# Kernel tuning notes

Measured on AMD Instinct MI355X. Metric: run time of the kernel, lower is better.

Reference implementation:

```python
import jax, jax.numpy as jnp
import numpy as np
from jax import lax

EPS = 1e-5
QUANT_BITS = 16  # Conv2dShift default input fixed-point bits


def round_fixed(x, quant_bits=QUANT_BITS):
    # fixed-point rounding of activations with straight-through estimator
    scale = 2.0 ** (quant_bits - 1)
    xq = jnp.round(x * scale) / scale
    return x + lax.stop_gradient(xq - x)


def shift_conv3x3(x, w_shift, stride=1):
    # w_shift already holds sign * 2^shift power-of-two weights (see setup)
    x = round_fixed(x)
    return lax.conv_general_dilated(
        x, w_shift, window_strides=(stride, stride), padding=[(1, 1), (1, 1)],
        dimension_numbers=("NCHW", "OIHW", "NCHW"))


def adder_conv3x3(x, w):
    # AdderNet: out[n,co,h,w] = -sum_{ci,kh,kw} |patch - w[co,ci,kh,kw]|
    Co = w.shape[0]
    # patches: [N, C*3*3, H, W], feature ordering (c, kh, kw) matches w.reshape
    p = lax.conv_general_dilated_patches(
        x, filter_shape=(3, 3), window_strides=(1, 1), padding=[(1, 1), (1, 1)])
    wf = w.reshape(Co, -1)

    def per_out_channel(wc):  # wc: [C*9]
        return -jnp.sum(jnp.abs(p - wc[None, :, None, None]), axis=1)  # [N,H,W]

    out = lax.map(per_out_channel, wf)  # [Co, N, H, W] (sequential: bounds memory)
    return jnp.transpose(out, (1, 0, 2, 3))


def batch_norm(x, gamma, beta):
    # training-mode BN (batch statistics), matching nn.BatchNorm2d default forward
    m = jnp.mean(x, axis=(0, 2, 3), keepdims=True)
    v = jnp.var(x, axis=(0, 2, 3), keepdims=True)
    xn = (x - m) * lax.rsqrt(v + EPS)
    return xn * gamma.reshape(1, -1, 1, 1) + beta.reshape(1, -1, 1, 1)


def _quantize_shift_weights(w, weight_bits=5):
    # DeepShift PS: weight -> sign * 2^round(log2|w|), shift clipped
    sign = jnp.where(w >= 0, 1.0, -1.0)
    shift = jnp.round(jnp.log2(jnp.abs(w) + 1e-12))
    shift = jnp.clip(shift, -(2.0 ** (weight_bits - 1) - 1.0), 0.0)
    return sign * jnp.exp2(shift)


def setup_inputs() -> dict:
    key = jax.random.key(0)
    ks = jax.random.split(key, 9)
    N, C, H, W = 64, 128, 32, 32
    planes = 128
    fan = 1.0 / np.sqrt(C * 9)
    x = jax.random.normal(ks[0], (N, C, H, W), dtype=jnp.float32)
    w_shift1 = _quantize_shift_weights(
        jax.random.normal(ks[1], (planes, C, 3, 3), dtype=jnp.float32) * fan)
    w_add1 = jax.random.normal(ks[2], (planes, planes, 3, 3), dtype=jnp.float32) * fan
    w_shift2 = _quantize_shift_weights(
        jax.random.normal(ks[3], (planes, planes, 3, 3), dtype=jnp.float32) * fan)
    w_add2 = jax.random.normal(ks[4], (planes, planes, 3, 3), dtype=jnp.float32) * fan
    gamma1 = jnp.ones((planes,), jnp.float32)
    beta1 = jnp.zeros((planes,), jnp.float32)
    gamma2 = jnp.ones((planes,), jnp.float32)
    beta2 = jnp.zeros((planes,), jnp.float32)
    return {"x": x, "w_shift1": w_shift1, "w_add1": w_add1, "gamma1": gamma1,
            "beta1": beta1, "w_shift2": w_shift2, "w_add2": w_add2,
            "gamma2": gamma2, "beta2": beta2}


def reference(x, w_shift1, w_add1, gamma1, beta1, w_shift2, w_add2, gamma2, beta2):
    residual = x
    out = shift_conv3x3(x, w_shift1, stride=1)
    out = adder_conv3x3(out, w_add1)
    out = jax.nn.relu(batch_norm(out, gamma1, beta1))
    out = shift_conv3x3(out, w_shift2, stride=1)
    out = adder_conv3x3(out, w_add2)
    out = batch_norm(out, gamma2, beta2)
    out = jax.nn.relu(out + residual)
    return out
```

## Files before the change

kernel.cpp:

```cpp
#include <hip/hip_runtime.h>


#define NB   64
#define CIN  128
#define HW   32
#define COUT 128
constexpr int PLANE    = HW * HW;
constexpr int NPAIR    = CIN / 2;
constexpr int CI_CHUNK = 4;
constexpr int CO_CHUNK = 8;
constexpr int LPLANE   = 34 * 32;
constexpr int LDS_TOT  = 2 * CI_CHUNK * LPLANE;
constexpr int A_CO     = 4;
constexpr float FSCALE    = 32768.0f;
constexpr float INV_SCALE = 1.0f / 32768.0f;
constexpr float QS     = 2048.0f;
constexpr float QB     = 32768.5f;
constexpr float INV_QS = 1.0f / 2048.0f;
constexpr unsigned PZ  = 0x80008000u;

constexpr int G_ROWB   = 32 * 4 * 16;
constexpr int G_CIQB   = 34 * G_ROWB;
constexpr int G_NB     = 4 * G_CIQB;

typedef _Float16 f16x8 __attribute__((ext_vector_type(8)));
typedef float    f32x4 __attribute__((ext_vector_type(4)));

#define GLOBAL_AS __attribute__((address_space(1)))
#define LDS_AS    __attribute__((address_space(3)))

__device__ __forceinline__ int fsw(int w) { return (w & 3) ^ ((w >> 2) & 3); }

__device__ __forceinline__ void gload_lds16(const void* g, void* l) {
    __builtin_amdgcn_global_load_lds((const GLOBAL_AS void*)g, (LDS_AS void*)l,
                                     16, 0, 0);
}
__device__ __forceinline__ float dpp_prev(float x) {
    return __int_as_float(__builtin_amdgcn_update_dpp(
        0, __float_as_int(x), 0x111, 0xF, 0xF, true));
}
__device__ __forceinline__ float dpp_next(float x) {
    return __int_as_float(__builtin_amdgcn_update_dpp(
        0, __float_as_int(x), 0x101, 0xF, 0xF, true));
}
__device__ __forceinline__ unsigned dpp_prev_u(unsigned x) {
    return (unsigned)__builtin_amdgcn_update_dpp(0, (int)x, 0x111, 0xF, 0xF, true);
}
__device__ __forceinline__ unsigned dpp_next_u(unsigned x) {
    return (unsigned)__builtin_amdgcn_update_dpp(0, (int)x, 0x101, 0xF, 0xF, true);
}
__device__ __forceinline__ uint4 dpp4_shr(uint4 v) {
    uint4 r;
    r.x = dpp_prev_u(v.x); r.y = dpp_prev_u(v.y);
    r.z = dpp_prev_u(v.z); r.w = dpp_prev_u(v.w);
    return r;
}
__device__ __forceinline__ uint4 dpp4_shl(uint4 v) {
    uint4 r;
    r.x = dpp_next_u(v.x); r.y = dpp_next_u(v.y);
    r.z = dpp_next_u(v.z); r.w = dpp_next_u(v.w);
    return r;
}
__device__ __forceinline__ void stage_plane4(const void* src, void* dst, int lane) {
#pragma unroll
    for (int i = 0; i < 4; ++i)
        gload_lds16((const char*)src + i * 1024 + lane * 16,
                    (char*)dst + 128 + i * 1024);
}
__device__ __forceinline__ unsigned q16(float a) {
    float t = fmaf(a, QS, QB);
    t = fminf(fmaxf(t, 0.0f), 65535.0f);
    return (unsigned)t;
}
__device__ __forceinline__ unsigned short f16b(float v) {
    return __builtin_bit_cast(unsigned short, (_Float16)v);
}

template <int WITH_BN>
__global__ __launch_bounds__(256) void transform_split(
    const float* __restrict__ in, const float* __restrict__ scale,
    const float* __restrict__ bias, uint4* __restrict__ G)
{
    __shared__ float sT[32 * 132];
    const int tid = threadIdx.x;
    const int b   = blockIdx.x;
    const int n   = b >> 5;
    const int ciq = (b >> 3) & 3;
    const int rq  = b & 7;

#pragma unroll
    for (int it = 0; it < 4; ++it) {
        int flat = it * 256 + tid;
        int ci_rel = flat >> 5;
        int px4 = (flat & 31) * 4;
        const float* ap = in + ((size_t)(n * CIN + ciq * 32 + ci_rel)) * PLANE
                             + rq * 128 + px4;
        float4 v = *reinterpret_cast<const float4*>(ap);
        if (WITH_BN) {
            float sc = scale[ciq * 32 + ci_rel], bs = bias[ciq * 32 + ci_rel];
            v.x = fmaxf(fmaf(v.x, sc, bs), 0.0f);
            v.y = fmaxf(fmaf(v.y, sc, bs), 0.0f);
            v.z = fmaxf(fmaf(v.z, sc, bs), 0.0f);
            v.w = fmaxf(fmaf(v.w, sc, bs), 0.0f);
        }
        v.x = rintf(v.x * FSCALE) * INV_SCALE;
        v.y = rintf(v.y * FSCALE) * INV_SCALE;
        v.z = rintf(v.z * FSCALE) * INV_SCALE;
        v.w = rintf(v.w * FSCALE) * INV_SCALE;
        *reinterpret_cast<float4*>(&sT[ci_rel * 132 + px4]) = v;
    }
    __syncthreads();

    uint4* Gp = G + ((size_t)n * G_NB + ciq * G_CIQB) / 16;
#pragma unroll
    for (int it = 0; it < 2; ++it) {
        int f = it * 256 + tid;
        int row_loc = f >> 7;
        int rem = f & 127;
        int w  = rem >> 2;
        int sg = rem & 3;
        int g  = sg ^ fsw(w);
        uint4 u;
        unsigned* up = &u.x;
#pragma unroll
        for (int j2 = 0; j2 < 4; ++j2) {
            unsigned lo = f16b(sT[(g * 8 + 2 * j2)     * 132 + row_loc * 32 + w]);
            unsigned hi = f16b(sT[(g * 8 + 2 * j2 + 1) * 132 + row_loc * 32 + w]);
            up[j2] = lo | (hi << 16);
        }
        int gr = rq * 4 + row_loc + 1;
        Gp[(gr * 32 + w) * 4 + sg] = u;
    }
    if (rq == 0 && tid < 128) Gp[tid] = make_uint4(0, 0, 0, 0);
    if (rq == 7 && tid < 128) Gp[33 * 128 + tid] = make_uint4(0, 0, 0, 0);
}

__global__ __launch_bounds__(256) void prep_weights(
    const float* __restrict__ a1, const float* __restrict__ a2,
    const float* __restrict__ s1w, const float* __restrict__ s2w,
    unsigned* __restrict__ wqo, unsigned* __restrict__ WFd,
    double* __restrict__ st)
{
    int i = blockIdx.x * 256 + threadIdx.x;
    if (blockIdx.x == 0) {
        st[threadIdx.x] = 0.0; st[threadIdx.x + 256] = 0.0;
    }
    if (i < 147456) {
        int layer = i >= 73728;
        int j   = i - layer * 73728;
        int co  = j / 576;
        int rem = j - co * 576;
        int cp  = rem / 9;
        int tap = rem - cp * 9;
        const float* w = layer ? a2 : a1;
        float f0 = w[((size_t)co * CIN + 2 * cp) * 9 + tap];
        float f1 = w[((size_t)co * CIN + 2 * cp + 1) * 9 + tap];
        wqo[i] = q16(f0) | (q16(f1) << 16);
    } else {
        int j = i - 147456;
        int layer = j >= 73728;
        int idx = j - layer * 73728;
        int j2  = idx & 3;
        int l   = (idx >> 2) & 63;
        int cot = (idx >> 8) & 7;
        int ciq = (idx >> 11) & 3;
        int tap = idx >> 13;
        int ci  = ciq * 32 + (l >> 4) * 8 + j2 * 2;
        int co  = cot * 16 + (l & 15);
        const float* w = layer ? s2w : s1w;
        unsigned lo = f16b(w[((size_t)co * CIN + ci) * 9 + tap]);
        unsigned hi = f16b(w[((size_t)co * CIN + ci + 1) * 9 + tap]);
        WFd[layer * 73728 + idx] = lo | (hi << 16);
    }
}

__global__ __launch_bounds__(256, 2) void conv_mfma(
    const uint4* __restrict__ G, const uint4* __restrict__ WF,
    unsigned* __restrict__ P)
{
    __shared__ uint4 sA[3072];
    const int tid  = threadIdx.x;
    const int lane = tid & 63;
    const int wid  = tid >> 6;
    const int b    = (blockIdx.x & 7) * 64 + (blockIdx.x >> 3);
    const int n    = b >> 3;
    const int q4   = b & 7;
    const int gsg  = lane >> 4;

    char* myL = (char*)sA + wid * 12288;
    const char* src = (const char*)G + (size_t)n * G_NB + (size_t)q4 * 4 * G_ROWB
                    + wid * 2048;

    f32x4 acc[8][2];
#pragma unroll
    for (int i = 0; i < 8; ++i)
#pragma unroll
        for (int j = 0; j < 2; ++j) acc[i][j] = (f32x4){0.f, 0.f, 0.f, 0.f};

    auto stage = [&](int ciq, int buf) {
        const char* s = src + ciq * G_CIQB;
#pragma unroll
        for (int rr = 0; rr < 3; ++rr)
#pragma unroll
            for (int k = 0; k < 2; ++k)
                gload_lds16(s + rr * 2048 + k * 1024 + lane * 16,
                            myL + buf * 6144 + rr * 2048 + k * 1024);
    };

    stage(0, 0);
    for (int ciq = 0; ciq < 4; ++ciq) {
        const int buf = ciq & 1;
        if (ciq < 3) {
            stage(ciq + 1, buf ^ 1);
            asm volatile("s_waitcnt vmcnt(6)" ::: "memory");
        } else {
            asm volatile("s_waitcnt vmcnt(0)" ::: "memory");
        }
        __builtin_amdgcn_sched_barrier(0);

        uint4 Brow[2][3];
        int pwh[2];
#pragma unroll
        for (int half = 0; half < 2; ++half) {
            pwh[half] = half * 16 + (lane & 15);
#pragma unroll
            for (int rr = 0; rr < 3; ++rr)
                Brow[half][rr] = *reinterpret_cast<const uint4*>(
                    myL + buf * 6144 + rr * 2048 + pwh[half] * 64
                    + ((gsg ^ fsw(pwh[half])) * 16));
        }
#pragma unroll
        for (int dh = 0; dh < 3; ++dh)
#pragma unroll
        for (int dw = 0; dw < 3; ++dw) {
            const uint4* wfp = WF + ((size_t)((dh * 3 + dw) * 4 + ciq)) * 512 + lane;
            f16x8 a[8];
#pragma unroll
            for (int cot = 0; cot < 8; ++cot)
                a[cot] = __builtin_bit_cast(f16x8, wfp[cot * 64]);
#pragma unroll
            for (int half = 0; half < 2; ++half) {
                uint4 braw;
                if (dw == 1) {
                    braw = Brow[half][dh];
                } else if (dw == 0) {
                    if (half == 0) braw = dpp4_shr(Brow[0][dh]);
                    else {
                        int w2 = pwh[1] - 1;
                        braw = *reinterpret_cast<const uint4*>(
                            myL + buf * 6144 + dh * 2048 + w2 * 64
                            + ((gsg ^ fsw(w2)) * 16));
                    }
                } else {
                    if (half == 1) braw = dpp4_shl(Brow[1][dh]);
                    else {
                        int w2 = pwh[0] + 1;
                        braw = *reinterpret_cast<const uint4*>(
                            myL + buf * 6144 + dh * 2048 + w2 * 64
                            + ((gsg ^ fsw(w2)) * 16));
                    }
                }
                f16x8 bf = __builtin_bit_cast(f16x8, braw);
#pragma unroll
                for (int cot = 0; cot < 8; ++cot)
                    acc[cot][half] = __builtin_amdgcn_mfma_f32_16x16x32_f16(
                        a[cot], bf, acc[cot][half], 0, 0, 0);
            }
        }
    }

    unsigned* Pn = P + (size_t)n * NPAIR * PLANE;
    const int r = q4 * 4 + wid;
#pragma unroll
    for (int cot = 0; cot < 8; ++cot) {
        int cp = cot * 8 + (lane >> 4) * 2;
#pragma unroll
        for (int p = 0; p < 2; ++p) {
            int px = r * 32 + p * 16 + (lane & 15);
            unsigned u01 = q16(acc[cot][p][0]) | (q16(acc[cot][p][1]) << 16);
            unsigned u23 = q16(acc[cot][p][2]) | (q16(acc[cot][p][3]) << 16);
            Pn[cp * PLANE + px] = u01;
            Pn[(cp + 1) * PLANE + px] = u23;
        }
    }
}

__global__ __launch_bounds__(256, 2) void conv_shift_valu(
    const float* __restrict__ in, const float* __restrict__ wgt,
    unsigned* __restrict__ out)
{
    __shared__ __align__(16) float sIn[LDS_TOT];
    const int tid  = threadIdx.x;
    const int lane = tid & 63;
    const int wid  = tid >> 6;
    const int bid  = (blockIdx.x & 7) * 128 + (blockIdx.x >> 3);
    const int n    = bid >> 4;
    const int co0  = (bid & 15) * CO_CHUNK;
    const int r    = tid >> 3;
    const int c    = tid & 7;
    const int c0   = c * 4;
    const bool cz  = (c == 0), c7 = (c == 7);

    float acc[4][CO_CHUNK];
#pragma unroll
    for (int p = 0; p < 4; ++p)
#pragma unroll
        for (int co = 0; co < CO_CHUNK; ++co) acc[p][co] = 0.0f;

    const float* inN = in + (size_t)n * CIN * PLANE;
    for (int idx = tid; idx < 512; idx += 256) {
        int slot = idx >> 6, wq = idx & 63;
        sIn[slot * LPLANE + (wq < 32 ? wq : 1024 + wq)] = 0.0f;
    }
    stage_plane4(inN + wid * PLANE, sIn + wid * LPLANE, lane);
    __syncthreads();

    int cur = 0;
    for (int ci0 = 0; ci0 < CIN; ci0 += CI_CHUNK) {
        if (ci0 + CI_CHUNK < CIN)
            stage_plane4(inN + (size_t)(ci0 + CI_CHUNK + wid) * PLANE,
                         sIn + ((cur ^ 1) * CI_CHUNK + wid) * LPLANE, lane);
        const float* sb = sIn + cur * CI_CHUNK * LPLANE;
#pragma unroll
        for (int cc = 0; cc < CI_CHUNK; ++cc) {
            float w[3][6];
#pragma unroll
            for (int dh = 0; dh < 3; ++dh) {
                const float* sp = sb + cc * LPLANE + (r + dh) * 32 + c0;
                float4 qv = *reinterpret_cast<const float4*>(sp);
                qv.x = rintf(qv.x * FSCALE) * INV_SCALE;
                qv.y = rintf(qv.y * FSCALE) * INV_SCALE;
                qv.z = rintf(qv.z * FSCALE) * INV_SCALE;
                qv.w = rintf(qv.w * FSCALE) * INV_SCALE;
                float lf = dpp_prev(qv.w);
                float rt = dpp_next(qv.x);
                w[dh][0] = cz ? 0.0f : lf;
                w[dh][1] = qv.x; w[dh][2] = qv.y; w[dh][3] = qv.z; w[dh][4] = qv.w;
                w[dh][5] = c7 ? 0.0f : rt;
            }
            const float* wp = wgt + ((size_t)co0 * CIN + (ci0 + cc)) * 9;
#pragma unroll
            for (int co = 0; co < CO_CHUNK; ++co)
#pragma unroll
                for (int dh = 0; dh < 3; ++dh)
#pragma unroll
                    for (int dw = 0; dw < 3; ++dw) {
                        const float wvv = wp[(size_t)co * CIN * 9 + dh * 3 + dw];
#pragma unroll
                        for (int p = 0; p < 4; ++p)
                            acc[p][co] = fmaf(w[dh][p + dw], wvv, acc[p][co]);
                    }
        }
        __syncthreads();
        cur ^= 1;
    }
    unsigned* outP = out + ((size_t)n * NPAIR + co0 / 2) * PLANE + r * HW + c0;
#pragma unroll
    for (int pr = 0; pr < CO_CHUNK / 2; ++pr) {
        uint4 v;
        unsigned* vp = &v.x;
#pragma unroll
        for (int p = 0; p < 4; ++p)
            vp[p] = q16(acc[p][2 * pr]) | (q16(acc[p][2 * pr + 1]) << 16);
        *reinterpret_cast<uint4*>(&outP[pr * PLANE]) = v;
    }
}

__global__ __launch_bounds__(256) void bn_relu_inplace(
    float4* __restrict__ io, const float* __restrict__ scale,
    const float* __restrict__ bias)
{
    int i = blockIdx.x * 256 + threadIdx.x;
    int c = (i >> 8) & 127;
    float sc = scale[c], bs = bias[c];
    float4 v = io[i];
    v.x = fmaxf(fmaf(v.x, sc, bs), 0.0f);
    v.y = fmaxf(fmaf(v.y, sc, bs), 0.0f);
    v.z = fmaxf(fmaf(v.z, sc, bs), 0.0f);
    v.w = fmaxf(fmaf(v.w, sc, bs), 0.0f);
    io[i] = v;
}

__global__ __launch_bounds__(256, 8) void adder_packed(
    const unsigned* __restrict__ in, const unsigned* __restrict__ wq,
    float* __restrict__ out, double* __restrict__ ssum, double* __restrict__ ssq)
{
    __shared__ __align__(16) unsigned sIn[4 * LPLANE];
    const int tid  = threadIdx.x;
    const int lane = tid & 63;
    const int wid  = tid >> 6;
    const int bid  = (blockIdx.x & 7) * 256 + (blockIdx.x >> 3);
    const int n    = bid >> 5;
    const int co0  = (bid & 31) * A_CO;
    const int r    = tid >> 3;
    const int c    = tid & 7;
    const int c0   = c * 4;
    const bool cz  = (c == 0), c7 = (c == 7);
    const unsigned pz = PZ;

    {
        int slot = tid >> 6, wqi = tid & 63;
        sIn[slot * LPLANE + (wqi < 32 ? wqi : 1024 + wqi)] = pz;
    }

    unsigned acc[4][A_CO];
#pragma unroll
    for (int p = 0; p < 4; ++p)
#pragma unroll
        for (int co = 0; co < A_CO; ++co) acc[p][co] = 0u;

    const unsigned* inN = in + (size_t)n * NPAIR * PLANE;

    stage_plane4(inN + (size_t)wid * PLANE, sIn + wid * LPLANE, lane);
    __syncthreads();

    int cur = 0;
    for (int s = 0; s < NPAIR / 2; ++s) {
        if (s >= 1 && s + 1 < NPAIR / 2 && wid < 2)
            stage_plane4(inN + (size_t)(2 * (s + 1) + wid) * PLANE,
                         sIn + ((cur ^ 1) * 2 + wid) * LPLANE, lane);

        const unsigned* sb = sIn + cur * 2 * LPLANE;
#pragma unroll
        for (int cc = 0; cc < 2; ++cc) {
            unsigned wi[3][6];
#pragma unroll
            for (int dh = 0; dh < 3; ++dh) {
                const unsigned* sp = sb + cc * LPLANE + (r + dh) * 32 + c0;
                uint4 qv = *reinterpret_cast<const uint4*>(sp);
                unsigned lf = dpp_prev_u(qv.w);
                unsigned rt = dpp_next_u(qv.x);
                wi[dh][0] = cz ? pz : lf;
                wi[dh][1] = qv.x; wi[dh][2] = qv.y; wi[dh][3] = qv.z; wi[dh][4] = qv.w;
                wi[dh][5] = c7 ? pz : rt;
            }
            const int cp = 2 * s + cc;
            const unsigned* wrow = wq + ((size_t)co0 * NPAIR + cp) * 9;
#pragma unroll
            for (int co = 0; co < A_CO; ++co)
#pragma unroll
                for (int dh = 0; dh < 3; ++dh)
#pragma unroll
                    for (int dw = 0; dw < 3; ++dw) {
                        const unsigned wv =
                            wrow[(size_t)co * NPAIR * 9 + dh * 3 + dw];
#pragma unroll
                        for (int p = 0; p < 4; ++p)
                            asm("v_sad_u16 %0, %1, %2, %0"
                                : "+v"(acc[p][co])
                                : "v"(wi[dh][p + dw]), "s"(wv));
                    }
        }
        __syncthreads();
        cur ^= 1;
    }

    float* outP = out + ((size_t)n * COUT + co0) * PLANE + r * HW + c0;
#pragma unroll
    for (int co = 0; co < A_CO; ++co) {
        float y0 = -(float)acc[0][co] * INV_QS;
        float y1 = -(float)acc[1][co] * INV_QS;
        float y2 = -(float)acc[2][co] * INV_QS;
        float y3 = -(float)acc[3][co] * INV_QS;
        *reinterpret_cast<float4*>(&outP[co * PLANE]) = make_float4(y0, y1, y2, y3);
        float s = (y0 + y1) + (y2 + y3);
        float q = fmaf(y0, y0, y1 * y1) + fmaf(y2, y2, y3 * y3);
#pragma unroll
        for (int m = 32; m > 0; m >>= 1) {
            s += __shfl_xor(s, m, 64);
            q += __shfl_xor(q, m, 64);
        }
        if (lane == 0) {
            atomicAdd(&ssum[co0 + co], (double)s);
            atomicAdd(&ssq [co0 + co], (double)q);
        }
    }
}

__global__ void finalize_bn(const double* __restrict__ ssum, const double* __restrict__ ssq,
                            const float* __restrict__ gamma, const float* __restrict__ beta,
                            float* __restrict__ scale, float* __restrict__ bias)
{
    int c = threadIdx.x;
    const double cnt = (double)NB * PLANE;
    double m   = ssum[c] / cnt;
    double var = ssq[c] / cnt - m * m;
    double rstd = 1.0 / sqrt(var + 1e-5);
    float sc = (float)((double)gamma[c] * rstd);
    scale[c] = sc;
    bias[c]  = beta[c] - (float)m * sc;
}

__global__ __launch_bounds__(256) void bn_add_relu(
    float4* __restrict__ io, const float4* __restrict__ res,
    const float* __restrict__ scale, const float* __restrict__ bias)
{
    int i = blockIdx.x * 256 + threadIdx.x;
    int c = (i >> 8) & 127;
    float sc = scale[c], bs = bias[c];
    float4 v = io[i];
    float4 x = res[i];
    v.x = fmaxf(fmaf(v.x, sc, bs) + x.x, 0.0f);
    v.y = fmaxf(fmaf(v.y, sc, bs) + x.y, 0.0f);
    v.z = fmaxf(fmaf(v.z, sc, bs) + x.z, 0.0f);
    v.w = fmaxf(fmaf(v.w, sc, bs) + x.w, 0.0f);
    io[i] = v;
}

extern "C" void kernel_launch(void* const* d_in, const int* in_sizes, int n_in,
                              void* d_out, int out_size, void* d_ws, size_t ws_size,
                              hipStream_t stream)
{
    const float* x    = (const float*)d_in[0];
    const float* wS1  = (const float*)d_in[1];
    const float* wA1  = (const float*)d_in[2];
    const float* g1   = (const float*)d_in[3];
    const float* b1   = (const float*)d_in[4];
    const float* wS2  = (const float*)d_in[5];
    const float* wA2  = (const float*)d_in[6];
    const float* g2   = (const float*)d_in[7];
    const float* b2   = (const float*)d_in[8];
    float* outp = (float*)d_out;

    char* ws = (char*)d_ws;
    const size_t MFMA_WS = 35788800;
    const bool mf = ws_size >= MFMA_WS;

    unsigned* P = (unsigned*)ws;
    double* st; float* sb; unsigned* wq; char* Gb = nullptr; unsigned* WF = nullptr;
    if (mf) {
        Gb = ws + 16777216;
        st = (double*)(ws + 34603008);
        sb = (float*)(ws + 34607104);
        wq = (unsigned*)(ws + 34609152);
        WF = (unsigned*)(ws + 35198976);
    } else {
        st = (double*)(ws + 16777216);
        sb = (float*)(st + 512);
        wq = (unsigned*)(sb + 512);
    }
    double* s1 = st,       *q1 = st + 128;
    double* s2 = st + 256, *q2 = st + 384;
    float* sc1 = sb,       *bi1 = sb + 128;
    float* sc2 = sb + 256, *bi2 = sb + 384;

    const int adderGrid = NB * (COUT / A_CO);
    const int ewGrid    = (NB * COUT * PLANE / 4) / 256;

    if (mf) {
        prep_weights<<<1152, 256, 0, stream>>>(wA1, wA2, wS1, wS2, wq, WF, st);
        transform_split<0><<<2048, 256, 0, stream>>>(x, nullptr, nullptr, (uint4*)Gb);
        conv_mfma<<<512, 256, 0, stream>>>((const uint4*)Gb, (const uint4*)WF, P);
        adder_packed<<<adderGrid, 256, 0, stream>>>(P, wq, outp, s1, q1);
        finalize_bn<<<1, 128, 0, stream>>>(s1, q1, g1, b1, sc1, bi1);
        transform_split<1><<<2048, 256, 0, stream>>>(outp, sc1, bi1, (uint4*)Gb);
        conv_mfma<<<512, 256, 0, stream>>>((const uint4*)Gb,
                                           (const uint4*)WF + 18432, P);
        adder_packed<<<adderGrid, 256, 0, stream>>>(P, wq + 73728, outp, s2, q2);
        finalize_bn<<<1, 128, 0, stream>>>(s2, q2, g2, b2, sc2, bi2);
        bn_add_relu<<<ewGrid, 256, 0, stream>>>((float4*)outp, (const float4*)x,
                                                sc2, bi2);
    } else {
        prep_weights<<<1152, 256, 0, stream>>>(wA1, wA2, wS1, wS2, wq,
                                               (unsigned*)ws, st);
        conv_shift_valu<<<1024, 256, 0, stream>>>(x, wS1, P);
        adder_packed<<<adderGrid, 256, 0, stream>>>(P, wq, outp, s1, q1);
        finalize_bn<<<1, 128, 0, stream>>>(s1, q1, g1, b1, sc1, bi1);
        bn_relu_inplace<<<ewGrid, 256, 0, stream>>>((float4*)outp, sc1, bi1);
        conv_shift_valu<<<1024, 256, 0, stream>>>(outp, wS2, P);
        adder_packed<<<adderGrid, 256, 0, stream>>>(P, wq + 73728, outp, s2, q2);
        finalize_bn<<<1, 128, 0, stream>>>(s2, q2, g2, b2, sc2, bi2);
        bn_add_relu<<<ewGrid, 256, 0, stream>>>((float4*)outp, (const float4*)x,
                                                sc2, bi2);
    }
}
```

Before: 420.7 us.

## Fuse weight prep and BN finalize into neighbors; restage adder input via registers

The weight-prep kernel is folded into the first transform_split launch as extra blocks, and the BN finalize kernels are removed by computing scale and bias inline in transform_split and bn_add_relu. This cuts several small launches and the serialization gaps between them. The adder kernel now double-buffers input planes through registers into a padded LDS layout with zero halo columns, replacing the DPP neighbor exchange with plain LDS reads. In exchange, BN statistics are recomputed in every block or thread, and the LDS row stride changes, which may alter bank-conflict behavior.

```diff
diff --git a/kernel.cpp b/kernel.cpp
--- a/kernel.cpp
+++ b/kernel.cpp
@@ -12,6 +12,7 @@
 constexpr int LPLANE   = 34 * 32;
 constexpr int LDS_TOT  = 2 * CI_CHUNK * LPLANE;
 constexpr int A_CO     = 4;
+constexpr int ASTRIDE  = 36;
 constexpr float FSCALE    = 32768.0f;
 constexpr float INV_SCALE = 1.0f / 32768.0f;
 constexpr float QS     = 2048.0f;
@@ -78,15 +79,68 @@
 
 template <int WITH_BN>
 __global__ __launch_bounds__(256) void transform_split(
-    const float* __restrict__ in, const float* __restrict__ scale,
-    const float* __restrict__ bias, uint4* __restrict__ G)
+    const float* __restrict__ in,
+    const double* __restrict__ st, const float* __restrict__ gamma,
+    const float* __restrict__ beta, uint4* __restrict__ G,
+    const float* __restrict__ a1, const float* __restrict__ a2,
+    const float* __restrict__ s1w, const float* __restrict__ s2w,
+    unsigned* __restrict__ wqo, unsigned* __restrict__ WFd,
+    double* __restrict__ stz)
 {
     __shared__ float sT[32 * 132];
+    __shared__ float sSC[32], sBI[32];
     const int tid = threadIdx.x;
     const int b   = blockIdx.x;
+
+    if (!WITH_BN && b >= 2048) {
+        if (b == 2048) { stz[tid] = 0.0; stz[tid + 256] = 0.0; }
+        int i = (b - 2048) * 256 + tid;
+        if (i < 147456) {
+            int layer = i >= 73728;
+            int j   = i - layer * 73728;
+            int co  = j / 576;
+            int rem = j - co * 576;
+            int cp  = rem / 9;
+            int tap = rem - cp * 9;
+            const float* w = layer ? a2 : a1;
+            float f0 = w[((size_t)co * CIN + 2 * cp) * 9 + tap];
+            float f1 = w[((size_t)co * CIN + 2 * cp + 1) * 9 + tap];
+            wqo[i] = q16(f0) | (q16(f1) << 16);
+        } else {
+            int j = i - 147456;
+            int layer = j >= 73728;
+            int idx = j - layer * 73728;
+            int j2  = idx & 3;
+            int l   = (idx >> 2) & 63;
+            int cot = (idx >> 8) & 7;
+            int ciq = (idx >> 11) & 3;
+            int tap = idx >> 13;
+            int ci  = ciq * 32 + (l >> 4) * 8 + j2 * 2;
+            int co  = cot * 16 + (l & 15);
+            const float* w = layer ? s2w : s1w;
+            unsigned lo = f16b(w[((size_t)co * CIN + ci) * 9 + tap]);
+            unsigned hi = f16b(w[((size_t)co * CIN + ci + 1) * 9 + tap]);
+            WFd[layer * 73728 + idx] = lo | (hi << 16);
+        }
+        return;
+    }
+
     const int n   = b >> 5;
     const int ciq = (b >> 3) & 3;
     const int rq  = b & 7;
+
+    if (WITH_BN) {
+        if (tid < 32) {
+            int ch = ciq * 32 + tid;
+            double m   = st[ch] / 65536.0;
+            double var = st[128 + ch] / 65536.0 - m * m;
+            double rstd = 1.0 / sqrt(var + 1e-5);
+            float sc = (float)((double)gamma[ch] * rstd);
+            sSC[tid] = sc;
+            sBI[tid] = beta[ch] - (float)m * sc;
+        }
+        __syncthreads();
+    }
 
 #pragma unroll
     for (int it = 0; it < 4; ++it) {
@@ -97,7 +151,7 @@
                              + rq * 128 + px4;
         float4 v = *reinterpret_cast<const float4*>(ap);
         if (WITH_BN) {
-            float sc = scale[ciq * 32 + ci_rel], bs = bias[ciq * 32 + ci_rel];
+            float sc = sSC[ci_rel], bs = sBI[ci_rel];
             v.x = fmaxf(fmaf(v.x, sc, bs), 0.0f);
             v.y = fmaxf(fmaf(v.y, sc, bs), 0.0f);
             v.z = fmaxf(fmaf(v.z, sc, bs), 0.0f);
@@ -133,45 +187,6 @@
     }
     if (rq == 0 && tid < 128) Gp[tid] = make_uint4(0, 0, 0, 0);
     if (rq == 7 && tid < 128) Gp[33 * 128 + tid] = make_uint4(0, 0, 0, 0);
-}
-
-__global__ __launch_bounds__(256) void prep_weights(
-    const float* __restrict__ a1, const float* __restrict__ a2,
-    const float* __restrict__ s1w, const float* __restrict__ s2w,
-    unsigned* __restrict__ wqo, unsigned* __restrict__ WFd,
-    double* __restrict__ st)
-{
-    int i = blockIdx.x * 256 + threadIdx.x;
-    if (blockIdx.x == 0) {
-        st[threadIdx.x] = 0.0; st[threadIdx.x + 256] = 0.0;
-    }
-    if (i < 147456) {
-        int layer = i >= 73728;
-        int j   = i - layer * 73728;
-        int co  = j / 576;
-        int rem = j - co * 576;
-        int cp  = rem / 9;
-        int tap = rem - cp * 9;
-        const float* w = layer ? a2 : a1;
-        float f0 = w[((size_t)co * CIN + 2 * cp) * 9 + tap];
-        float f1 = w[((size_t)co * CIN + 2 * cp + 1) * 9 + tap];
-        wqo[i] = q16(f0) | (q16(f1) << 16);
-    } else {
-        int j = i - 147456;
-        int layer = j >= 73728;
-        int idx = j - layer * 73728;
-        int j2  = idx & 3;
-        int l   = (idx >> 2) & 63;
-        int cot = (idx >> 8) & 7;
-        int ciq = (idx >> 11) & 3;
-        int tap = idx >> 13;
-        int ci  = ciq * 32 + (l >> 4) * 8 + j2 * 2;
-        int co  = cot * 16 + (l & 15);
-        const float* w = layer ? s2w : s1w;
-        unsigned lo = f16b(w[((size_t)co * CIN + ci) * 9 + tap]);
-        unsigned hi = f16b(w[((size_t)co * CIN + ci + 1) * 9 + tap]);
-        WFd[layer * 73728 + idx] = lo | (hi << 16);
-    }
 }
 
 __global__ __launch_bounds__(256, 2) void conv_mfma(
@@ -385,22 +400,31 @@
     const unsigned* __restrict__ in, const unsigned* __restrict__ wq,
     float* __restrict__ out, double* __restrict__ ssum, double* __restrict__ ssq)
 {
-    __shared__ __align__(16) unsigned sIn[4 * LPLANE];
+    __shared__ __align__(16) unsigned sRaw[4 + 133 * ASTRIDE];
+    unsigned* sL = sRaw + 4;
     const int tid  = threadIdx.x;
     const int lane = tid & 63;
-    const int wid  = tid >> 6;
     const int bid  = (blockIdx.x & 7) * 256 + (blockIdx.x >> 3);
     const int n    = bid >> 5;
     const int co0  = (bid & 31) * A_CO;
     const int r    = tid >> 3;
-    const int c    = tid & 7;
-    const int c0   = c * 4;
-    const bool cz  = (c == 0), c7 = (c == 7);
+    const int c0   = (tid & 7) * 4;
     const unsigned pz = PZ;
 
-    {
-        int slot = tid >> 6, wqi = tid & 63;
-        sIn[slot * LPLANE + (wqi < 32 ? wqi : 1024 + wqi)] = pz;
+    for (int i = tid; i < 696; i += 256) {
+        int addr;
+        if (i < 4) {
+            addr = i - 4;
+        } else if (i < 184) {
+            int j = i - 4;
+            addr = (j / 36) * 33 * ASTRIDE + (j % 36);
+        } else {
+            int j = i - 184;
+            int dr = j >> 2, col = 32 + (j & 3);
+            int s = dr >> 5, rr = dr & 31;
+            addr = (s * 33 + 1 + rr) * ASTRIDE + col;
+        }
+        sL[addr] = pz;
     }
 
     unsigned acc[4][A_CO];
@@ -409,30 +433,30 @@
 #pragma unroll
         for (int co = 0; co < A_CO; ++co) acc[p][co] = 0u;
 
-    const unsigned* inN = in + (size_t)n * NPAIR * PLANE;
-
-    stage_plane4(inN + (size_t)wid * PLANE, sIn + wid * LPLANE, lane);
+    const uint4* inN4 = (const uint4*)(in + (size_t)n * NPAIR * PLANE);
+
+    auto wslot = [&](int sl, uint4 v) {
+        *reinterpret_cast<uint4*>(&sL[(sl * 33 + 1 + r) * ASTRIDE + c0]) = v;
+    };
+
+    uint4 rg0 = inN4[tid], rg1 = inN4[256 + tid];
+    wslot(0, rg0); wslot(1, rg1);
+    rg0 = inN4[512 + tid]; rg1 = inN4[768 + tid];
     __syncthreads();
 
-    int cur = 0;
     for (int s = 0; s < NPAIR / 2; ++s) {
-        if (s >= 1 && s + 1 < NPAIR / 2 && wid < 2)
-            stage_plane4(inN + (size_t)(2 * (s + 1) + wid) * PLANE,
-                         sIn + ((cur ^ 1) * 2 + wid) * LPLANE, lane);
-
-        const unsigned* sb = sIn + cur * 2 * LPLANE;
+        const int bsl = (s & 1) * 2;
 #pragma unroll
         for (int cc = 0; cc < 2; ++cc) {
             unsigned wi[3][6];
 #pragma unroll
             for (int dh = 0; dh < 3; ++dh) {
-                const unsigned* sp = sb + cc * LPLANE + (r + dh) * 32 + c0;
-                uint4 qv = *reinterpret_cast<const uint4*>(sp);
-                unsigned lf = dpp_prev_u(qv.w);
-                unsigned rt = dpp_next_u(qv.x);
-                wi[dh][0] = cz ? pz : lf;
-                wi[dh][1] = qv.x; wi[dh][2] = qv.y; wi[dh][3] = qv.z; wi[dh][4] = qv.w;
-                wi[dh][5] = c7 ? pz : rt;
+                const unsigned* rowp = &sL[((bsl + cc) * 33 + r + dh) * ASTRIDE];
+                wi[dh][0] = rowp[c0 - 1];
+                uint4 qv = *reinterpret_cast<const uint4*>(&rowp[c0]);
+                wi[dh][1] = qv.x; wi[dh][2] = qv.y;
+                wi[dh][3] = qv.z; wi[dh][4] = qv.w;
+                wi[dh][5] = rowp[c0 + 4];
             }
             const int cp = 2 * s + cc;
             const unsigned* wrow = wq + ((size_t)co0 * NPAIR + cp) * 9;
@@ -451,8 +475,15 @@
                                 : "v"(wi[dh][p + dw]), "s"(wv));
                     }
         }
+        if (s + 1 < NPAIR / 2) {
+            const int tsl = ((s + 1) & 1) * 2;
+            wslot(tsl, rg0); wslot(tsl + 1, rg1);
+        }
+        if (s + 2 < NPAIR / 2) {
+            rg0 = inN4[(2 * s + 4) * 256 + tid];
+            rg1 = inN4[(2 * s + 5) * 256 + tid];
+        }
         __syncthreads();
-        cur ^= 1;
     }
 
     float* outP = out + ((size_t)n * COUT + co0) * PLANE + r * HW + c0;
@@ -477,6 +508,26 @@
     }
 }
 
+__global__ __launch_bounds__(256) void prep_weights(
+    const float* __restrict__ a1, const float* __restrict__ a2,
+    unsigned* __restrict__ wqo, double* __restrict__ st)
+{
+    int i = blockIdx.x * 256 + threadIdx.x;
+    if (blockIdx.x == 0) {
+        st[threadIdx.x] = 0.0; st[threadIdx.x + 256] = 0.0;
+    }
+    int layer = i >= 73728;
+    int j   = i - layer * 73728;
+    int co  = j / 576;
+    int rem = j - co * 576;
+    int cp  = rem / 9;
+    int tap = rem - cp * 9;
+    const float* w = layer ? a2 : a1;
+    float f0 = w[((size_t)co * CIN + 2 * cp) * 9 + tap];
+    float f1 = w[((size_t)co * CIN + 2 * cp + 1) * 9 + tap];
+    wqo[i] = q16(f0) | (q16(f1) << 16);
+}
+
 __global__ void finalize_bn(const double* __restrict__ ssum, const double* __restrict__ ssq,
                             const float* __restrict__ gamma, const float* __restrict__ beta,
                             float* __restrict__ scale, float* __restrict__ bias)
@@ -493,11 +544,16 @@
 
 __global__ __launch_bounds__(256) void bn_add_relu(
     float4* __restrict__ io, const float4* __restrict__ res,
-    const float* __restrict__ scale, const float* __restrict__ bias)
+    const double* __restrict__ st, const float* __restrict__ gamma,
+    const float* __restrict__ beta)
 {
     int i = blockIdx.x * 256 + threadIdx.x;
     int c = (i >> 8) & 127;
-    float sc = scale[c], bs = bias[c];
+    double m   = st[c] / 65536.0;
+    double var = st[128 + c] / 65536.0 - m * m;
+    double rstd = 1.0 / sqrt(var + 1e-5);
+    float sc = (float)((double)gamma[c] * rstd);
+    float bs = beta[c] - (float)m * sc;
     float4 v = io[i];
     float4 x = res[i];
     v.x = fmaxf(fmaf(v.x, sc, bs) + x.x, 0.0f);
@@ -548,29 +604,28 @@
     const int ewGrid    = (NB * COUT * PLANE / 4) / 256;
 
     if (mf) {
-        prep_weights<<<1152, 256, 0, stream>>>(wA1, wA2, wS1, wS2, wq, WF, st);
-        transform_split<0><<<2048, 256, 0, stream>>>(x, nullptr, nullptr, (uint4*)Gb);
+        transform_split<0><<<3200, 256, 0, stream>>>(
+            x, nullptr, nullptr, nullptr, (uint4*)Gb,
+            wA1, wA2, wS1, wS2, wq, WF, st);
         conv_mfma<<<512, 256, 0, stream>>>((const uint4*)Gb, (const uint4*)WF, P);
         adder_packed<<<adderGrid, 256, 0, stream>>>(P, wq, outp, s1, q1);
-        finalize_bn<<<1, 128, 0, stream>>>(s1, q1, g1, b1, sc1, bi1);
-        transform_split<1><<<2048, 256, 0, stream>>>(outp, sc1, bi1, (uint4*)Gb);
+        transform_split<1><<<2048, 256, 0, stream>>>(
+            outp, s1, g1, b1, (uint4*)Gb,
+            nullptr, nullptr, nullptr, nullptr, nullptr, nullptr, nullptr);
         conv_mfma<<<512, 256, 0, stream>>>((const uint4*)Gb,
                                            (const uint4*)WF + 18432, P);
         adder_packed<<<adderGrid, 256, 0, stream>>>(P, wq + 73728, outp, s2, q2);
-        finalize_bn<<<1, 128, 0, stream>>>(s2, q2, g2, b2, sc2, bi2);
         bn_add_relu<<<ewGrid, 256, 0, stream>>>((float4*)outp, (const float4*)x,
-                                                sc2, bi2);
+                                                s2, g2, b2);
     } else {
-        prep_weights<<<1152, 256, 0, stream>>>(wA1, wA2, wS1, wS2, wq,
-                                               (unsigned*)ws, st);
+        prep_weights<<<576, 256, 0, stream>>>(wA1, wA2, wq, st);
         conv_shift_valu<<<1024, 256, 0, stream>>>(x, wS1, P);
         adder_packed<<<adderGrid, 256, 0, stream>>>(P, wq, outp, s1, q1);
         finalize_bn<<<1, 128, 0, stream>>>(s1, q1, g1, b1, sc1, bi1);
         bn_relu_inplace<<<ewGrid, 256, 0, stream>>>((float4*)outp, sc1, bi1);
         conv_shift_valu<<<1024, 256, 0, stream>>>(outp, wS2, P);
         adder_packed<<<adderGrid, 256, 0, stream>>>(P, wq + 73728, outp, s2, q2);
-        finalize_bn<<<1, 128, 0, stream>>>(s2, q2, g2, b2, sc2, bi2);
         bn_add_relu<<<ewGrid, 256, 0, stream>>>((float4*)outp, (const float4*)x,
-                                                sc2, bi2);
-    }
-}
+                                                s2, g2, b2);
+    }
+}
```

New measurement: 423.4 us. About the same (+0.7%).
